# Kernel tuning notes

Hardware: AMD Instinct MI355X
Metric: run time of the kernel (lower is better)

## Reference

```python
import jax, jax.numpy as jnp
import numpy as np

INPUT_SIZE = 12288  # C*H*W = 3*64*64
HIDDEN = 1024
OUT_SHAPE = (3, 64, 64)
T_STEPS = 256


def setup_inputs() -> dict:
    key = jax.random.key(0)
    ks = jax.random.split(key, 7)
    s = 0.02
    frames = jax.random.normal(ks[0], (T_STEPS, *OUT_SHAPE), dtype=jnp.float32)
    W_ih = jax.random.normal(ks[1], (4 * HIDDEN, INPUT_SIZE), dtype=jnp.float32) * s
    W_hh = jax.random.normal(ks[2], (4 * HIDDEN, HIDDEN), dtype=jnp.float32) * s
    b_ih = jax.random.normal(ks[3], (4 * HIDDEN,), dtype=jnp.float32) * s
    b_hh = jax.random.normal(ks[4], (4 * HIDDEN,), dtype=jnp.float32) * s
    fc_w = jax.random.normal(ks[5], (INPUT_SIZE, HIDDEN), dtype=jnp.float32) * s
    fc_b = jax.random.normal(ks[6], (INPUT_SIZE,), dtype=jnp.float32) * s
    return {"frames": frames, "W_ih": W_ih, "W_hh": W_hh, "b_ih": b_ih,
            "b_hh": b_hh, "fc_w": fc_w, "fc_b": fc_b, "T": T_STEPS}


def _lstm_scan(x_flat, W_ih, W_hh, b_ih, b_hh):
    # Precompute input projections for all timesteps in one GEMM: (T, 4H)
    x_proj = x_flat @ W_ih.T + b_ih + b_hh
    H = W_hh.shape[1]

    def step(carry, xp):
        h, c = carry  # (H,), (H,)
        gates = xp + h @ W_hh.T  # (4H,)
        i = jax.nn.sigmoid(gates[0 * H:1 * H])
        f = jax.nn.sigmoid(gates[1 * H:2 * H])
        g = jnp.tanh(gates[2 * H:3 * H])
        o = jax.nn.sigmoid(gates[3 * H:4 * H])
        c_new = f * c + i * g
        h_new = o * jnp.tanh(c_new)
        return (h_new, c_new), None

    init = (jnp.zeros((H,), x_flat.dtype), jnp.zeros((H,), x_flat.dtype))
    (h_T, _), _ = jax.lax.scan(step, init, x_proj)
    return h_T


def reference(frames, W_ih, W_hh, b_ih, b_hh, fc_w, fc_b, T):
    Tn, C, Hh, Ww = frames.shape
    x_flat = frames.reshape(Tn, -1)  # (T, C*H*W)
    h_T = _lstm_scan(x_flat, W_ih, W_hh, b_ih, b_hh)  # (HIDDEN,)
    context = h_T @ fc_w.T + fc_b  # (C*H*W,)
    return context.reshape(1, C, Hh, Ww)
```

## Files before the change

### kernel.cpp

```cpp
#include <hip/hip_runtime.h>
#include <math.h>

#define K_IN 12288
#define HID  1024
#define G4   4096
#define TS   256
#define NKS  8
#define KSP  (K_IN / NKS)
#define NST  (KSP / 16)

typedef unsigned long long u64;
typedef unsigned int u32;
typedef __attribute__((ext_vector_type(4))) float f32x4;
typedef __attribute__((ext_vector_type(16))) float f32x16;
typedef __attribute__((ext_vector_type(8))) _Float16 half8;
typedef __attribute__((ext_vector_type(4))) _Float16 half4;

__global__ __launch_bounds__(512, 2) void xproj_gemm(
    const float* __restrict__ X,
    const float* __restrict__ W,
    float* __restrict__ xprojT)
{
  __shared__ __align__(16) _Float16 Ahi[2][128][8];
  __shared__ __align__(16) _Float16 Alo[2][128][8];
  __shared__ __align__(16) _Float16 Bhi[2][256][8];
  __shared__ __align__(16) _Float16 Blo[2][256][8];

  const int tid = threadIdx.x;
  const int wave = tid >> 6;
  const int lane = tid & 63;
  const int l31 = lane & 31;
  const int kh = lane >> 5;

  const int j0 = blockIdx.x * 128;
  const int kbeg = blockIdx.y * KSP;

  const int jw = (wave & 1) * 64;
  const int tw = (wave >> 1) * 64;

  const int wrow = tid >> 2;
  const int wkq  = tid & 3;
  const int xrow = tid >> 1;
  const int xkq  = tid & 1;

  const float* wsrc = W + (size_t)(j0 + wrow) * K_IN + kbeg + wkq * 4;
  const float* xsrc = X + (size_t)xrow * K_IN + kbeg + xkq * 8;

  f32x16 acc[2][2];
#pragma unroll
  for (int mi = 0; mi < 2; ++mi)
#pragma unroll
    for (int ni = 0; ni < 2; ++ni)
#pragma unroll
      for (int e = 0; e < 16; ++e) acc[mi][ni][e] = 0.f;

  f32x4 wvA  = *(const f32x4*)(wsrc);
  f32x4 xv0A = *(const f32x4*)(xsrc);
  f32x4 xv1A = *(const f32x4*)(xsrc + 4);
  f32x4 wvB  = *(const f32x4*)(wsrc + 16);
  f32x4 xv0B = *(const f32x4*)(xsrc + 16);
  f32x4 xv1B = *(const f32x4*)(xsrc + 16 + 4);

#define STAGE(WV, XV0, XV1)                                                  \
  {                                                                          \
    half4 hw, lw;                                                            \
    _Pragma("unroll")                                                        \
    for (int e = 0; e < 4; ++e) {                                            \
      _Float16 h = (_Float16)WV[e];                                          \
      hw[e] = h;                                                             \
      lw[e] = (_Float16)(WV[e] - (float)h);                                  \
    }                                                                        \
    *(half4*)&Ahi[wkq >> 1][wrow][(wkq & 1) * 4] = hw;                       \
    *(half4*)&Alo[wkq >> 1][wrow][(wkq & 1) * 4] = lw;                       \
    half8 hx, lx;                                                            \
    _Pragma("unroll")                                                        \
    for (int e = 0; e < 4; ++e) {                                            \
      _Float16 h0 = (_Float16)XV0[e];                                        \
      hx[e] = h0;                                                            \
      lx[e] = (_Float16)(XV0[e] - (float)h0);                                \
      _Float16 h1 = (_Float16)XV1[e];                                        \
      hx[e + 4] = h1;                                                        \
      lx[e + 4] = (_Float16)(XV1[e] - (float)h1);                            \
    }                                                                        \
    *(half8*)&Bhi[xkq][xrow][0] = hx;                                        \
    *(half8*)&Blo[xkq][xrow][0] = lx;                                        \
  }

#define COMPUTE()                                                            \
  {                                                                          \
    half8 aH[2], aL[2], bH[2], bL[2];                                        \
    _Pragma("unroll")                                                        \
    for (int mi = 0; mi < 2; ++mi) {                                         \
      aH[mi] = *(const half8*)&Ahi[kh][jw + mi * 32 + l31][0];               \
      aL[mi] = *(const half8*)&Alo[kh][jw + mi * 32 + l31][0];               \
    }                                                                        \
    _Pragma("unroll")                                                        \
    for (int ni = 0; ni < 2; ++ni) {                                         \
      bH[ni] = *(const half8*)&Bhi[kh][tw + ni * 32 + l31][0];               \
      bL[ni] = *(const half8*)&Blo[kh][tw + ni * 32 + l31][0];               \
    }                                                                        \
    acc[0][0] = __builtin_amdgcn_mfma_f32_32x32x16_f16(aH[0], bH[0], acc[0][0], 0, 0, 0); \
    acc[0][1] = __builtin_amdgcn_mfma_f32_32x32x16_f16(aH[0], bH[1], acc[0][1], 0, 0, 0); \
    acc[1][0] = __builtin_amdgcn_mfma_f32_32x32x16_f16(aH[1], bH[0], acc[1][0], 0, 0, 0); \
    acc[1][1] = __builtin_amdgcn_mfma_f32_32x32x16_f16(aH[1], bH[1], acc[1][1], 0, 0, 0); \
    acc[0][0] = __builtin_amdgcn_mfma_f32_32x32x16_f16(aH[0], bL[0], acc[0][0], 0, 0, 0); \
    acc[0][1] = __builtin_amdgcn_mfma_f32_32x32x16_f16(aH[0], bL[1], acc[0][1], 0, 0, 0); \
    acc[1][0] = __builtin_amdgcn_mfma_f32_32x32x16_f16(aH[1], bL[0], acc[1][0], 0, 0, 0); \
    acc[1][1] = __builtin_amdgcn_mfma_f32_32x32x16_f16(aH[1], bL[1], acc[1][1], 0, 0, 0); \
    acc[0][0] = __builtin_amdgcn_mfma_f32_32x32x16_f16(aL[0], bH[0], acc[0][0], 0, 0, 0); \
    acc[0][1] = __builtin_amdgcn_mfma_f32_32x32x16_f16(aL[0], bH[1], acc[0][1], 0, 0, 0); \
    acc[1][0] = __builtin_amdgcn_mfma_f32_32x32x16_f16(aL[1], bH[0], acc[1][0], 0, 0, 0); \
    acc[1][1] = __builtin_amdgcn_mfma_f32_32x32x16_f16(aL[1], bH[1], acc[1][1], 0, 0, 0); \
  }

  for (int s = 0; s < NST; s += 2) {
    STAGE(wvA, xv0A, xv1A);
    __syncthreads();
    if (s + 2 < NST) {
      const int ko = (s + 2) * 16;
      wvA  = *(const f32x4*)(wsrc + ko);
      xv0A = *(const f32x4*)(xsrc + ko);
      xv1A = *(const f32x4*)(xsrc + ko + 4);
    }
    COMPUTE();
    __syncthreads();
    STAGE(wvB, xv0B, xv1B);
    __syncthreads();
    if (s + 3 < NST) {
      const int ko = (s + 3) * 16;
      wvB  = *(const f32x4*)(wsrc + ko);
      xv0B = *(const f32x4*)(xsrc + ko);
      xv1B = *(const f32x4*)(xsrc + ko + 4);
    }
    COMPUTE();
    __syncthreads();
  }

#pragma unroll
  for (int mi = 0; mi < 2; ++mi)
#pragma unroll
    for (int ni = 0; ni < 2; ++ni)
#pragma unroll
      for (int rg = 0; rg < 16; ++rg) {
        const int j = j0 + jw + mi * 32 + (rg & 3) + 8 * (rg >> 2) + 4 * kh;
        const int t = tw + ni * 32 + l31;
        atomicAdd(&xprojT[(size_t)j * TS + t], acc[mi][ni][rg]);
      }
}

#define NWG 128
#define UPW 8

__global__ __launch_bounds__(256, 1) void lstm_scan(
    const float* __restrict__ W_hh,
    const float* __restrict__ xprojT,
    const float* __restrict__ b_ih, const float* __restrict__ b_hh,
    u64* __restrict__ hmsg)
{
  const int tid = threadIdx.x;
  const int w = blockIdx.x;
  const int u0 = w * UPW;
  const int r = tid >> 3;
  const int sub = tid & 7;
  const int gate = r >> 3;
  const int uu = r & 7;
  const int hrow = gate * HID + u0 + uu;

  __shared__ __align__(16) float h_lds[8 * 132];
  __shared__ float gates_lds[32];
  __shared__ float c_lds[UPW];

  float4 Wreg[32];
  const float4* wp = (const float4*)(W_hh + (size_t)hrow * HID + sub * 128);
#pragma unroll
  for (int i = 0; i < 32; ++i) Wreg[i] = wp[i];

  const float* xrow = xprojT + (size_t)hrow * TS;
  const float bias = b_ih[hrow] + b_hh[hrow];

  if (tid < UPW) c_lds[tid] = 0.f;
  __syncthreads();

  for (int t = 0; t < TS; ++t) {
    float xp = 0.f;
    if (sub == 0) xp = xrow[t] + bias;

    float p0 = 0.f, p1 = 0.f, p2 = 0.f, p3 = 0.f;
    if (t > 0) {
      const u64* slot = hmsg + (t & 1) * HID;
      const u32 tt = (u32)t;
      u64 m0, m1, m2, m3;
      do {
        m0 = __hip_atomic_load(&slot[tid * 4 + 0], __ATOMIC_RELAXED,
                               __HIP_MEMORY_SCOPE_AGENT);
      } while ((u32)(m0 >> 32) != tt);
      m1 = __hip_atomic_load(&slot[tid * 4 + 1], __ATOMIC_RELAXED,
                             __HIP_MEMORY_SCOPE_AGENT);
      m2 = __hip_atomic_load(&slot[tid * 4 + 2], __ATOMIC_RELAXED,
                             __HIP_MEMORY_SCOPE_AGENT);
      m3 = __hip_atomic_load(&slot[tid * 4 + 3], __ATOMIC_RELAXED,
                             __HIP_MEMORY_SCOPE_AGENT);
      while ((u32)(m1 >> 32) != tt)
        m1 = __hip_atomic_load(&slot[tid * 4 + 1], __ATOMIC_RELAXED,
                               __HIP_MEMORY_SCOPE_AGENT);
      while ((u32)(m2 >> 32) != tt)
        m2 = __hip_atomic_load(&slot[tid * 4 + 2], __ATOMIC_RELAXED,
                               __HIP_MEMORY_SCOPE_AGENT);
      while ((u32)(m3 >> 32) != tt)
        m3 = __hip_atomic_load(&slot[tid * 4 + 3], __ATOMIC_RELAXED,
                               __HIP_MEMORY_SCOPE_AGENT);
      __syncthreads();
      const int st = tid >> 5;
      const int off = (tid & 31) * 4;
      h_lds[st * 132 + off + 0] = __uint_as_float((u32)m0);
      h_lds[st * 132 + off + 1] = __uint_as_float((u32)m1);
      h_lds[st * 132 + off + 2] = __uint_as_float((u32)m2);
      h_lds[st * 132 + off + 3] = __uint_as_float((u32)m3);
      __syncthreads();
      const float4* hl = (const float4*)(h_lds + sub * 132);
#pragma unroll
      for (int i = 0; i < 32; i += 4) {
        float4 h4;
        h4 = hl[i + 0];
        p0 += Wreg[i + 0].x * h4.x + Wreg[i + 0].y * h4.y +
              Wreg[i + 0].z * h4.z + Wreg[i + 0].w * h4.w;
        h4 = hl[i + 1];
        p1 += Wreg[i + 1].x * h4.x + Wreg[i + 1].y * h4.y +
              Wreg[i + 1].z * h4.z + Wreg[i + 1].w * h4.w;
        h4 = hl[i + 2];
        p2 += Wreg[i + 2].x * h4.x + Wreg[i + 2].y * h4.y +
              Wreg[i + 2].z * h4.z + Wreg[i + 2].w * h4.w;
        h4 = hl[i + 3];
        p3 += Wreg[i + 3].x * h4.x + Wreg[i + 3].y * h4.y +
              Wreg[i + 3].z * h4.z + Wreg[i + 3].w * h4.w;
      }
    }
    float partial = (p0 + p1) + (p2 + p3);
    partial += __shfl_xor(partial, 1, 64);
    partial += __shfl_xor(partial, 2, 64);
    partial += __shfl_xor(partial, 4, 64);
    if (sub == 0) {
      float gsum = partial + xp;
      float act = (gate == 2) ? tanhf(gsum) : 1.f / (1.f + expf(-gsum));
      gates_lds[gate * 8 + uu] = act;
    }
    __syncthreads();
    if (tid < UPW) {
      float iv = gates_lds[0 * 8 + tid];
      float fv = gates_lds[1 * 8 + tid];
      float gv = gates_lds[2 * 8 + tid];
      float ov = gates_lds[3 * 8 + tid];
      float c = fv * c_lds[tid] + iv * gv;
      c_lds[tid] = c;
      float hnew = ov * tanhf(c);
      u64 msg = ((u64)(u32)(t + 1) << 32) | (u64)__float_as_uint(hnew);
      __hip_atomic_store(&hmsg[((t + 1) & 1) * HID + u0 + tid], msg,
                         __ATOMIC_RELAXED, __HIP_MEMORY_SCOPE_AGENT);
    }
  }
}

__global__ __launch_bounds__(256) void fc_kernel(
    const float* __restrict__ fc_w,
    const float* __restrict__ fc_b,
    const u64* __restrict__ hmsg,
    float* __restrict__ out)
{
  __shared__ float h_s[HID];
  const int tid = threadIdx.x;
  for (int k = tid; k < HID; k += 256)
    h_s[k] = __uint_as_float((u32)hmsg[k]);
  __syncthreads();
  const int r = tid >> 2;
  const int sub = tid & 3;
  const int j = blockIdx.x * 64 + r;
  const float4* wrow = (const float4*)(fc_w + (size_t)j * HID + sub * 256);
  const float4* hp = (const float4*)(h_s + sub * 256);
  float s = 0.f;
#pragma unroll
  for (int i = 0; i < 64; ++i) {
    float4 wv = wrow[i];
    float4 hv = hp[i];
    s += wv.x * hv.x + wv.y * hv.y + wv.z * hv.z + wv.w * hv.w;
  }
  s += __shfl_xor(s, 1, 64);
  s += __shfl_xor(s, 2, 64);
  if (sub == 0) out[j] = s + fc_b[j];
}

extern "C" void kernel_launch(void* const* d_in, const int* in_sizes, int n_in,
                              void* d_out, int out_size, void* d_ws, size_t ws_size,
                              hipStream_t stream) {
  const float* frames = (const float*)d_in[0];
  const float* W_ih   = (const float*)d_in[1];
  const float* W_hh   = (const float*)d_in[2];
  const float* b_ih   = (const float*)d_in[3];
  const float* b_hh   = (const float*)d_in[4];
  const float* fc_w   = (const float*)d_in[5];
  const float* fc_b   = (const float*)d_in[6];
  float* out = (float*)d_out;

  const size_t XPROJ_BYTES = (size_t)TS * G4 * 4;
  char* ws = (char*)d_ws;
  float* xprojT = (float*)ws;
  u64*   hmsg   = (u64*)(ws + XPROJ_BYTES);

  hipMemsetAsync(xprojT, 0, XPROJ_BYTES, stream);
  xproj_gemm<<<dim3(G4 / 128, NKS), 512, 0, stream>>>(frames, W_ih, xprojT);
  lstm_scan<<<dim3(NWG), 256, 0, stream>>>(W_hh, xprojT, b_ih, b_hh, hmsg);
  fc_kernel<<<dim3(12288 / 64), 256, 0, stream>>>(fc_w, fc_b, hmsg, out);
}
```

Before: 1.083 ms.

## Double-buffer and swizzle GEMM LDS, replace atomics with split-K partial reduce

The x-projection GEMM now double-buffers its LDS tiles so staging the next K-slice overlaps the MFMA compute on the current one. It also XOR-swizzles the LDS offsets to reduce bank conflicts, and halves the number of barriers per iteration. When workspace allows, the split-K partials are written to separate buffers and summed (plus bias) by a new reduce kernel, replacing the memset and atomicAdd traffic. Otherwise bias is pre-initialised into the accumulator. The scan loop's dot product is also simplified to a single accumulator, which lengthens its dependency chain.

```diff
diff --git a/kernel.cpp b/kernel.cpp
--- a/kernel.cpp
+++ b/kernel.cpp
@@ -19,12 +19,13 @@
 __global__ __launch_bounds__(512, 2) void xproj_gemm(
     const float* __restrict__ X,
     const float* __restrict__ W,
-    float* __restrict__ xprojT)
-{
-  __shared__ __align__(16) _Float16 Ahi[2][128][8];
-  __shared__ __align__(16) _Float16 Alo[2][128][8];
-  __shared__ __align__(16) _Float16 Bhi[2][256][8];
-  __shared__ __align__(16) _Float16 Blo[2][256][8];
+    float* __restrict__ outp,
+    int atomic_mode)
+{
+  __shared__ __align__(16) _Float16 Ah[2][2][128][8];
+  __shared__ __align__(16) _Float16 Al[2][2][128][8];
+  __shared__ __align__(16) _Float16 Bh[2][2][256][8];
+  __shared__ __align__(16) _Float16 Bl[2][2][256][8];
 
   const int tid = threadIdx.x;
   const int wave = tid >> 6;
@@ -46,6 +47,17 @@
   const float* wsrc = W + (size_t)(j0 + wrow) * K_IN + kbeg + wkq * 4;
   const float* xsrc = X + (size_t)xrow * K_IN + kbeg + xkq * 8;
 
+  const int khw = wkq >> 1;
+  const int a_woff = khw * 1024 + ((wrow * 8) ^ (khw * 32)) + (wkq & 1) * 4;
+  const int b_woff = xkq * 2048 + ((xrow * 8) ^ (xkq * 32));
+  int a_roff[2], b_roff[2];
+#pragma unroll
+  for (int mi = 0; mi < 2; ++mi)
+    a_roff[mi] = kh * 1024 + (((jw + mi * 32 + l31) * 8) ^ (kh * 32));
+#pragma unroll
+  for (int ni = 0; ni < 2; ++ni)
+    b_roff[ni] = kh * 2048 + (((tw + ni * 32 + l31) * 8) ^ (kh * 32));
+
   f32x16 acc[2][2];
 #pragma unroll
   for (int mi = 0; mi < 2; ++mi)
@@ -54,14 +66,7 @@
 #pragma unroll
       for (int e = 0; e < 16; ++e) acc[mi][ni][e] = 0.f;
 
-  f32x4 wvA  = *(const f32x4*)(wsrc);
-  f32x4 xv0A = *(const f32x4*)(xsrc);
-  f32x4 xv1A = *(const f32x4*)(xsrc + 4);
-  f32x4 wvB  = *(const f32x4*)(wsrc + 16);
-  f32x4 xv0B = *(const f32x4*)(xsrc + 16);
-  f32x4 xv1B = *(const f32x4*)(xsrc + 16 + 4);
-
-#define STAGE(WV, XV0, XV1)                                                  \
+#define STAGE(BUF, WV, XV0, XV1)                                             \
   {                                                                          \
     half4 hw, lw;                                                            \
     _Pragma("unroll")                                                        \
@@ -70,8 +75,8 @@
       hw[e] = h;                                                             \
       lw[e] = (_Float16)(WV[e] - (float)h);                                  \
     }                                                                        \
-    *(half4*)&Ahi[wkq >> 1][wrow][(wkq & 1) * 4] = hw;                       \
-    *(half4*)&Alo[wkq >> 1][wrow][(wkq & 1) * 4] = lw;                       \
+    *(half4*)(&Ah[BUF][0][0][0] + a_woff) = hw;                              \
+    *(half4*)(&Al[BUF][0][0][0] + a_woff) = lw;                              \
     half8 hx, lx;                                                            \
     _Pragma("unroll")                                                        \
     for (int e = 0; e < 4; ++e) {                                            \
@@ -82,22 +87,22 @@
       hx[e + 4] = h1;                                                        \
       lx[e + 4] = (_Float16)(XV1[e] - (float)h1);                            \
     }                                                                        \
-    *(half8*)&Bhi[xkq][xrow][0] = hx;                                        \
-    *(half8*)&Blo[xkq][xrow][0] = lx;                                        \
-  }
-
-#define COMPUTE()                                                            \
+    *(half8*)(&Bh[BUF][0][0][0] + b_woff) = hx;                              \
+    *(half8*)(&Bl[BUF][0][0][0] + b_woff) = lx;                              \
+  }
+
+#define COMPUTE(BUF)                                                         \
   {                                                                          \
     half8 aH[2], aL[2], bH[2], bL[2];                                        \
     _Pragma("unroll")                                                        \
     for (int mi = 0; mi < 2; ++mi) {                                         \
-      aH[mi] = *(const half8*)&Ahi[kh][jw + mi * 32 + l31][0];               \
-      aL[mi] = *(const half8*)&Alo[kh][jw + mi * 32 + l31][0];               \
+      aH[mi] = *(const half8*)(&Ah[BUF][0][0][0] + a_roff[mi]);              \
+      aL[mi] = *(const half8*)(&Al[BUF][0][0][0] + a_roff[mi]);              \
     }                                                                        \
     _Pragma("unroll")                                                        \
     for (int ni = 0; ni < 2; ++ni) {                                         \
-      bH[ni] = *(const half8*)&Bhi[kh][tw + ni * 32 + l31][0];               \
-      bL[ni] = *(const half8*)&Blo[kh][tw + ni * 32 + l31][0];               \
+      bH[ni] = *(const half8*)(&Bh[BUF][0][0][0] + b_roff[ni]);              \
+      bL[ni] = *(const half8*)(&Bl[BUF][0][0][0] + b_roff[ni]);              \
     }                                                                        \
     acc[0][0] = __builtin_amdgcn_mfma_f32_32x32x16_f16(aH[0], bH[0], acc[0][0], 0, 0, 0); \
     acc[0][1] = __builtin_amdgcn_mfma_f32_32x32x16_f16(aH[0], bH[1], acc[0][1], 0, 0, 0); \
@@ -113,18 +118,24 @@
     acc[1][1] = __builtin_amdgcn_mfma_f32_32x32x16_f16(aL[1], bH[1], acc[1][1], 0, 0, 0); \
   }
 
+  f32x4 wvA  = *(const f32x4*)(wsrc);
+  f32x4 xv0A = *(const f32x4*)(xsrc);
+  f32x4 xv1A = *(const f32x4*)(xsrc + 4);
+  f32x4 wvB  = *(const f32x4*)(wsrc + 16);
+  f32x4 xv0B = *(const f32x4*)(xsrc + 16);
+  f32x4 xv1B = *(const f32x4*)(xsrc + 16 + 4);
+
+  STAGE(0, wvA, xv0A, xv1A);
+  __syncthreads();
+  {
+    wvA  = *(const f32x4*)(wsrc + 32);
+    xv0A = *(const f32x4*)(xsrc + 32);
+    xv1A = *(const f32x4*)(xsrc + 32 + 4);
+  }
+
   for (int s = 0; s < NST; s += 2) {
-    STAGE(wvA, xv0A, xv1A);
-    __syncthreads();
-    if (s + 2 < NST) {
-      const int ko = (s + 2) * 16;
-      wvA  = *(const f32x4*)(wsrc + ko);
-      xv0A = *(const f32x4*)(xsrc + ko);
-      xv1A = *(const f32x4*)(xsrc + ko + 4);
-    }
-    COMPUTE();
-    __syncthreads();
-    STAGE(wvB, xv0B, xv1B);
+    STAGE(1, wvB, xv0B, xv1B);
+    COMPUTE(0);
     __syncthreads();
     if (s + 3 < NST) {
       const int ko = (s + 3) * 16;
@@ -132,10 +143,18 @@
       xv0B = *(const f32x4*)(xsrc + ko);
       xv1B = *(const f32x4*)(xsrc + ko + 4);
     }
-    COMPUTE();
+    if (s + 2 < NST) STAGE(0, wvA, xv0A, xv1A);
+    COMPUTE(1);
     __syncthreads();
-  }
-
+    if (s + 4 < NST) {
+      const int ko = (s + 4) * 16;
+      wvA  = *(const f32x4*)(wsrc + ko);
+      xv0A = *(const f32x4*)(xsrc + ko);
+      xv1A = *(const f32x4*)(xsrc + ko + 4);
+    }
+  }
+
+  float* dst = atomic_mode ? outp : outp + (size_t)blockIdx.y * G4 * TS;
 #pragma unroll
   for (int mi = 0; mi < 2; ++mi)
 #pragma unroll
@@ -144,8 +163,34 @@
       for (int rg = 0; rg < 16; ++rg) {
         const int j = j0 + jw + mi * 32 + (rg & 3) + 8 * (rg >> 2) + 4 * kh;
         const int t = tw + ni * 32 + l31;
-        atomicAdd(&xprojT[(size_t)j * TS + t], acc[mi][ni][rg]);
+        if (atomic_mode) atomicAdd(&dst[(size_t)j * TS + t], acc[mi][ni][rg]);
+        else             dst[(size_t)j * TS + t] = acc[mi][ni][rg];
       }
+}
+
+__global__ __launch_bounds__(256) void xproj_reduce(
+    const float* __restrict__ xpartT, int nks,
+    const float* __restrict__ b_ih, const float* __restrict__ b_hh,
+    float* __restrict__ xprojT)
+{
+  const int idx = (blockIdx.x * 256 + threadIdx.x) * 4;
+  float4 s = *(const float4*)(xpartT + idx);
+  for (int ks = 1; ks < nks; ++ks) {
+    float4 p = *(const float4*)(xpartT + (size_t)ks * G4 * TS + idx);
+    s.x += p.x; s.y += p.y; s.z += p.z; s.w += p.w;
+  }
+  const int j = idx >> 8;
+  const float bias = b_ih[j] + b_hh[j];
+  s.x += bias; s.y += bias; s.z += bias; s.w += bias;
+  *(float4*)(xprojT + idx) = s;
+}
+
+__global__ __launch_bounds__(256) void bias_init(
+    const float* __restrict__ b_ih, const float* __restrict__ b_hh,
+    float* __restrict__ xprojT)
+{
+  const int j = blockIdx.x;
+  xprojT[(size_t)j * TS + threadIdx.x] = b_ih[j] + b_hh[j];
 }
 
 #define NWG 128
@@ -154,7 +199,6 @@
 __global__ __launch_bounds__(256, 1) void lstm_scan(
     const float* __restrict__ W_hh,
     const float* __restrict__ xprojT,
-    const float* __restrict__ b_ih, const float* __restrict__ b_hh,
     u64* __restrict__ hmsg)
 {
   const int tid = threadIdx.x;
@@ -176,16 +220,15 @@
   for (int i = 0; i < 32; ++i) Wreg[i] = wp[i];
 
   const float* xrow = xprojT + (size_t)hrow * TS;
-  const float bias = b_ih[hrow] + b_hh[hrow];
 
   if (tid < UPW) c_lds[tid] = 0.f;
   __syncthreads();
 
   for (int t = 0; t < TS; ++t) {
     float xp = 0.f;
-    if (sub == 0) xp = xrow[t] + bias;
-
-    float p0 = 0.f, p1 = 0.f, p2 = 0.f, p3 = 0.f;
+    if (sub == 0) xp = xrow[t];
+
+    float partial = 0.f;
     if (t > 0) {
       const u64* slot = hmsg + (t & 1) * HID;
       const u32 tt = (u32)t;
@@ -219,23 +262,12 @@
       __syncthreads();
       const float4* hl = (const float4*)(h_lds + sub * 132);
 #pragma unroll
-      for (int i = 0; i < 32; i += 4) {
-        float4 h4;
-        h4 = hl[i + 0];
-        p0 += Wreg[i + 0].x * h4.x + Wreg[i + 0].y * h4.y +
-              Wreg[i + 0].z * h4.z + Wreg[i + 0].w * h4.w;
-        h4 = hl[i + 1];
-        p1 += Wreg[i + 1].x * h4.x + Wreg[i + 1].y * h4.y +
-              Wreg[i + 1].z * h4.z + Wreg[i + 1].w * h4.w;
-        h4 = hl[i + 2];
-        p2 += Wreg[i + 2].x * h4.x + Wreg[i + 2].y * h4.y +
-              Wreg[i + 2].z * h4.z + Wreg[i + 2].w * h4.w;
-        h4 = hl[i + 3];
-        p3 += Wreg[i + 3].x * h4.x + Wreg[i + 3].y * h4.y +
-              Wreg[i + 3].z * h4.z + Wreg[i + 3].w * h4.w;
+      for (int i = 0; i < 32; ++i) {
+        float4 h4 = hl[i];
+        partial += Wreg[i].x * h4.x + Wreg[i].y * h4.y +
+                   Wreg[i].z * h4.z + Wreg[i].w * h4.w;
       }
     }
-    float partial = (p0 + p1) + (p2 + p3);
     partial += __shfl_xor(partial, 1, 64);
     partial += __shfl_xor(partial, 2, 64);
     partial += __shfl_xor(partial, 4, 64);
@@ -300,13 +332,23 @@
   const float* fc_b   = (const float*)d_in[6];
   float* out = (float*)d_out;
 
-  const size_t XPROJ_BYTES = (size_t)TS * G4 * 4;
+  const size_t XB = (size_t)TS * G4 * 4;
   char* ws = (char*)d_ws;
   float* xprojT = (float*)ws;
-  u64*   hmsg   = (u64*)(ws + XPROJ_BYTES);
-
-  hipMemsetAsync(xprojT, 0, XPROJ_BYTES, stream);
-  xproj_gemm<<<dim3(G4 / 128, NKS), 512, 0, stream>>>(frames, W_ih, xprojT);
-  lstm_scan<<<dim3(NWG), 256, 0, stream>>>(W_hh, xprojT, b_ih, b_hh, hmsg);
-  fc_kernel<<<dim3(12288 / 64), 256, 0, stream>>>(fc_w, fc_b, hmsg, out);
-}
+  const bool xpart_path = ws_size >= XB * (1 + NKS) + (1 << 20);
+
+  if (xpart_path) {
+    float* xpartT = (float*)(ws + XB);
+    u64*   hmsg   = (u64*)(ws + XB * (1 + NKS));
+    xproj_gemm<<<dim3(G4 / 128, NKS), 512, 0, stream>>>(frames, W_ih, xpartT, 0);
+    xproj_reduce<<<dim3(G4 * TS / 4 / 256), 256, 0, stream>>>(xpartT, NKS, b_ih, b_hh, xprojT);
+    lstm_scan<<<dim3(NWG), 256, 0, stream>>>(W_hh, xprojT, hmsg);
+    fc_kernel<<<dim3(12288 / 64), 256, 0, stream>>>(fc_w, fc_b, hmsg, out);
+  } else {
+    u64* hmsg = (u64*)(ws + XB);
+    bias_init<<<dim3(G4), 256, 0, stream>>>(b_ih, b_hh, xprojT);
+    xproj_gemm<<<dim3(G4 / 128, NKS), 512, 0, stream>>>(frames, W_ih, xprojT, 1);
+    lstm_scan<<<dim3(NWG), 256, 0, stream>>>(W_hh, xprojT, hmsg);
+    fc_kernel<<<dim3(12288 / 64), 256, 0, stream>>>(fc_w, fc_b, hmsg, out);
+  }
+}
```

New measurement: 1.035 ms. -4.4%, faster.
